# Kernel tuning notes

Hardware: AMD Instinct MI355X
Metric: run time of the kernel (lower is better)

The kernel has to match this reference:

```python
import jax, jax.numpy as jnp
import numpy as np

N_SRC = [700000, 51200, 5120]
N_DST = [51200, 5120, 1024]
N_EDGE = [768000, 51200, 5120]
IN_FEATS, N_HIDDEN, N_CLASSES = 128, 256, 47


def setup_inputs() -> dict:
    key = jax.random.key(0)
    ks = jax.random.split(key, 16)
    inp = {}
    inp["x"] = jax.random.normal(ks[0], (N_SRC[0], IN_FEATS), dtype=jnp.float32)
    # edge lists per block: src indexes block-src nodes, dst indexes block-dst nodes
    for l in range(3):
        inp[f"src{l}"] = jax.random.randint(ks[1 + 2 * l], (N_EDGE[l],), 0, N_SRC[l], dtype=jnp.int32)
        inp[f"dst{l}"] = jax.random.randint(ks[2 + 2 * l], (N_EDGE[l],), 0, N_DST[l], dtype=jnp.int32)
    dims = [(IN_FEATS, N_HIDDEN), (N_HIDDEN, N_HIDDEN), (N_HIDDEN, N_CLASSES)]
    for l, (di, do) in enumerate(dims):
        scale = 1.0 / np.sqrt(di)
        inp[f"Ws{l}"] = jax.random.normal(ks[7 + 3 * l], (di, do), dtype=jnp.float32) * scale
        inp[f"Wn{l}"] = jax.random.normal(ks[8 + 3 * l], (di, do), dtype=jnp.float32) * scale
        inp[f"b{l}"] = jnp.zeros((do,), dtype=jnp.float32)
    return inp


def _sage_conv(h, src, dst, n_dst, Ws, Wn, b):
    # mean-aggregate neighbor (src) features onto dst nodes, then dual linear
    h_dst = h[:n_dst]                                   # dst nodes are a prefix of src nodes
    msg = jax.ops.segment_sum(h[src], dst, num_segments=n_dst)
    deg = jax.ops.segment_sum(jnp.ones((src.shape[0], 1), h.dtype), dst, num_segments=n_dst)
    h_neigh = msg / jnp.maximum(deg, 1.0)               # zero-degree dst -> 0 (DGL convention)
    return h_dst @ Ws + h_neigh @ Wn + b


def reference(x, src0, dst0, src1, dst1, src2, dst2,
              Ws0, Wn0, b0, Ws1, Wn1, b1, Ws2, Wn2, b2):
    h = _sage_conv(x, src0, dst0, N_DST[0], Ws0, Wn0, b0)
    h = jax.nn.relu(h)  # dropout = identity in eval
    h = _sage_conv(h, src1, dst1, N_DST[1], Ws1, Wn1, b1)
    h = jax.nn.relu(h)
    h = _sage_conv(h, src2, dst2, N_DST[2], Ws2, Wn2, b2)
    return h
```

## Files before the change

kernel.cpp:

```cpp
#include <hip/hip_runtime.h>


typedef __bf16 bf16x8 __attribute__((ext_vector_type(8)));
typedef float f32x4 __attribute__((ext_vector_type(4)));

static __device__ __forceinline__ unsigned short f32_to_bf16(float f) {
    unsigned u = __float_as_uint(f);
    u += 0x7fffu + ((u >> 16) & 1u);
    return (unsigned short)(u >> 16);
}
static __device__ __forceinline__ float bf16lo(unsigned u) { return __uint_as_float(u << 16); }
static __device__ __forceinline__ float bf16hi(unsigned u) { return __uint_as_float(u & 0xffff0000u); }

__global__ void sage_prep(const float* __restrict__ x, unsigned short* __restrict__ xcast,
                          const float* __restrict__ Ws0, const float* __restrict__ Wn0,
                          const float* __restrict__ Ws1, const float* __restrict__ Wn1,
                          const float* __restrict__ Ws2, const float* __restrict__ Wn2,
                          unsigned short* __restrict__ WT0, unsigned short* __restrict__ WT1,
                          unsigned short* __restrict__ WT2,
                          const int* __restrict__ d0, int* __restrict__ c0,
                          const int* __restrict__ d1, int* __restrict__ c1,
                          const int* __restrict__ d2, int* __restrict__ c2) {
    const int b = blockIdx.x;
    if (b < 6400) {
        int i = b * 256 + threadIdx.x;
        float4 v = ((const float4*)x)[i];
        uint2 o;
        o.x = (unsigned)f32_to_bf16(v.x) | ((unsigned)f32_to_bf16(v.y) << 16);
        o.y = (unsigned)f32_to_bf16(v.z) | ((unsigned)f32_to_bf16(v.w) << 16);
        ((uint2*)xcast)[i] = o;
    } else if (b < 6656) {
        int idx = (b - 6400) * 256 + threadIdx.x;
        int n = idx >> 8, k = idx & 255;
        float v = (k < 128) ? Ws0[(size_t)k * 256 + n] : Wn0[(size_t)(k - 128) * 256 + n];
        WT0[idx] = f32_to_bf16(v);
    } else if (b < 7168) {
        int idx = (b - 6656) * 256 + threadIdx.x;
        int n = idx >> 9, k = idx & 511;
        float v = (k < 256) ? Ws1[(size_t)k * 256 + n] : Wn1[(size_t)(k - 256) * 256 + n];
        WT1[idx] = f32_to_bf16(v);
    } else if (b < 7262) {
        int idx = (b - 7168) * 256 + threadIdx.x;
        int n = idx >> 9, k = idx & 511;
        float v = (k < 256) ? Ws2[(size_t)k * 47 + n] : Wn2[(size_t)(k - 256) * 47 + n];
        WT2[idx] = f32_to_bf16(v);
    } else if (b < 8762) {
        int i = (b - 7262) * 256 + threadIdx.x;
        int2 d = ((const int2*)d0)[i];
        atomicAdd(&c0[d.x], 1);
        atomicAdd(&c0[d.y], 1);
    } else if (b < 8862) {
        int i = (b - 8762) * 256 + threadIdx.x;
        int2 d = ((const int2*)d1)[i];
        atomicAdd(&c1[d.x], 1);
        atomicAdd(&c1[d.y], 1);
    } else {
        int i = (b - 8862) * 256 + threadIdx.x;
        int2 d = ((const int2*)d2)[i];
        atomicAdd(&c2[d.x], 1);
        atomicAdd(&c2[d.y], 1);
    }
}

__launch_bounds__(1024)
__global__ void sage_scan(const int* __restrict__ c0, int* __restrict__ o0, int* __restrict__ u0,
                          const int* __restrict__ c1, int* __restrict__ o1, int* __restrict__ u1,
                          const int* __restrict__ c2, int* __restrict__ o2, int* __restrict__ u2,
                          int* __restrict__ sync) {
    const int b = blockIdx.x;
    const int tid = threadIdx.x;
    const int lane = tid & 63;
    const int wid = tid >> 6;
    const int* counts; int* off; int* cur; int chunk, first, nblk, n;
    if (b < 50)      { counts = c0; off = o0; cur = u0; chunk = b;      first = 0;  nblk = 50; n = 51200; }
    else if (b < 55) { counts = c1; off = o1; cur = u1; chunk = b - 50; first = 50; nblk = 5;  n = 5120;  }
    else             { counts = c2; off = o2; cur = u2; chunk = 0;      first = 55; nblk = 1;  n = 1024;  }

    const int idx = chunk * 1024 + tid;
    const int v = counts[idx];

    int incl = v;
#pragma unroll
    for (int d = 1; d < 64; d <<= 1) {
        int t = __shfl_up(incl, d, 64);
        if (lane >= d) incl += t;
    }

    __shared__ int wsum[16];
    __shared__ int s_base;
    if (lane == 63) wsum[wid] = incl;
    __syncthreads();

    if (tid < 64) {
        int s = (lane < 16) ? wsum[lane] : 0;
        int inc = s;
#pragma unroll
        for (int d = 1; d < 16; d <<= 1) {
            int t = __shfl_up(inc, d, 64);
            if (lane >= d) inc += t;
        }
        if (lane < 16) wsum[lane] = inc - s;
        if (lane == 15) {
            __hip_atomic_store(&sync[16 + b], inc, __ATOMIC_RELEASE, __HIP_MEMORY_SCOPE_AGENT);
            __hip_atomic_fetch_add(&sync[0], 1, __ATOMIC_RELEASE, __HIP_MEMORY_SCOPE_AGENT);
        }
    }
    if (tid == 0) {
        while (__hip_atomic_load(&sync[0], __ATOMIC_ACQUIRE, __HIP_MEMORY_SCOPE_AGENT) < 56)
            __builtin_amdgcn_s_sleep(2);
    }
    __syncthreads();

    if (tid < 64) {
        int p = (lane < chunk)
            ? __hip_atomic_load(&sync[16 + first + lane], __ATOMIC_RELAXED, __HIP_MEMORY_SCOPE_AGENT)
            : 0;
#pragma unroll
        for (int d = 32; d >= 1; d >>= 1) p += __shfl_down(p, d, 64);
        if (lane == 0) s_base = p;
    }
    __syncthreads();

    const int excl = s_base + wsum[wid] + (incl - v);
    off[idx] = excl;
    cur[idx] = excl;
    if (chunk == nblk - 1 && tid == 1023) off[n] = excl + v;
}

__global__ void sage_fill(const int* __restrict__ s0, const int* __restrict__ d0,
                          int* __restrict__ u0, int* __restrict__ r0,
                          const int* __restrict__ s1, const int* __restrict__ d1,
                          int* __restrict__ u1, int* __restrict__ r1,
                          const int* __restrict__ s2, const int* __restrict__ d2,
                          int* __restrict__ u2, int* __restrict__ r2) {
    const int b = blockIdx.x;
    if (b < 1500) {
        int i = b * 256 + threadIdx.x;
        int2 s = ((const int2*)s0)[i];
        int2 d = ((const int2*)d0)[i];
        int p0 = atomicAdd(&u0[d.x], 1);
        int p1 = atomicAdd(&u0[d.y], 1);
        r0[p0] = s.x;
        r0[p1] = s.y;
    } else if (b < 1600) {
        int i = (b - 1500) * 256 + threadIdx.x;
        int2 s = ((const int2*)s1)[i];
        int2 d = ((const int2*)d1)[i];
        int p0 = atomicAdd(&u1[d.x], 1);
        int p1 = atomicAdd(&u1[d.y], 1);
        r1[p0] = s.x;
        r1[p1] = s.y;
    } else {
        int i = (b - 1600) * 256 + threadIdx.x;
        int2 s = ((const int2*)s2)[i];
        int2 d = ((const int2*)d2)[i];
        int p0 = atomicAdd(&u2[d.x], 1);
        int p1 = atomicAdd(&u2[d.y], 1);
        r2[p0] = s.x;
        r2[p1] = s.y;
    }
}

__global__ void sage_gather0(const float* __restrict__ x, const int* __restrict__ csr,
                             const int* __restrict__ off, unsigned short* __restrict__ out,
                             int n_dst) {
    int row = (blockIdx.x * 256 + threadIdx.x) >> 6;
    if (row >= n_dst) return;
    const int lane = threadIdx.x & 63;
    const int half = lane >> 5;
    const int fl = lane & 31;
    const int beg = off[row], end = off[row + 1];
    const float4* hp = (const float4*)x + fl;
    float4 accA = make_float4(0.f, 0.f, 0.f, 0.f);
    float4 accB = make_float4(0.f, 0.f, 0.f, 0.f);
    int i = beg;
    for (; i + 7 < end; i += 8) {
        int s0 = csr[i + half];
        int s1 = csr[i + 2 + half];
        int s2 = csr[i + 4 + half];
        int s3 = csr[i + 6 + half];
        float4 v0 = hp[(size_t)s0 * 32];
        float4 v1 = hp[(size_t)s1 * 32];
        float4 v2 = hp[(size_t)s2 * 32];
        float4 v3 = hp[(size_t)s3 * 32];
        accA.x += v0.x; accA.y += v0.y; accA.z += v0.z; accA.w += v0.w;
        accB.x += v1.x; accB.y += v1.y; accB.z += v1.z; accB.w += v1.w;
        accA.x += v2.x; accA.y += v2.y; accA.z += v2.z; accA.w += v2.w;
        accB.x += v3.x; accB.y += v3.y; accB.z += v3.z; accB.w += v3.w;
    }
    for (; i + 1 < end; i += 2) {
        int s = csr[i + half];
        float4 v = hp[(size_t)s * 32];
        accA.x += v.x; accA.y += v.y; accA.z += v.z; accA.w += v.w;
    }
    if (i < end && half == 0) {
        int s = csr[i];
        float4 v = hp[(size_t)s * 32];
        accA.x += v.x; accA.y += v.y; accA.z += v.z; accA.w += v.w;
    }
    accA.x += accB.x; accA.y += accB.y; accA.z += accB.z; accA.w += accB.w;
    accA.x += __shfl_down(accA.x, 32);
    accA.y += __shfl_down(accA.y, 32);
    accA.z += __shfl_down(accA.z, 32);
    accA.w += __shfl_down(accA.w, 32);
    if (half == 0) {
        float inv = 1.0f / fmaxf((float)(end - beg), 1.0f);
        uint2 o;
        o.x = (unsigned)f32_to_bf16(accA.x * inv) | ((unsigned)f32_to_bf16(accA.y * inv) << 16);
        o.y = (unsigned)f32_to_bf16(accA.z * inv) | ((unsigned)f32_to_bf16(accA.w * inv) << 16);
        ((uint2*)out)[(size_t)row * 32 + fl] = o;
    }
}

__global__ void sage_gather256(const unsigned short* __restrict__ h, const int* __restrict__ csr,
                               const int* __restrict__ off, unsigned short* __restrict__ out,
                               int n_dst) {
    int row = (blockIdx.x * 256 + threadIdx.x) >> 6;
    if (row >= n_dst) return;
    const int lane = threadIdx.x & 63;
    const int half = lane >> 5;
    const int fl = lane & 31;
    const int beg = off[row], end = off[row + 1];
    const uint4* hp = (const uint4*)h + fl;
    float a[8] = {0.f, 0.f, 0.f, 0.f, 0.f, 0.f, 0.f, 0.f};
    float b[8] = {0.f, 0.f, 0.f, 0.f, 0.f, 0.f, 0.f, 0.f};
    int i = beg;
    for (; i + 3 < end; i += 4) {
        int s0 = csr[i + half];
        int s1 = csr[i + 2 + half];
        uint4 u0 = hp[(size_t)s0 * 32];
        uint4 u1 = hp[(size_t)s1 * 32];
        a[0] += bf16lo(u0.x); a[1] += bf16hi(u0.x);
        a[2] += bf16lo(u0.y); a[3] += bf16hi(u0.y);
        a[4] += bf16lo(u0.z); a[5] += bf16hi(u0.z);
        a[6] += bf16lo(u0.w); a[7] += bf16hi(u0.w);
        b[0] += bf16lo(u1.x); b[1] += bf16hi(u1.x);
        b[2] += bf16lo(u1.y); b[3] += bf16hi(u1.y);
        b[4] += bf16lo(u1.z); b[5] += bf16hi(u1.z);
        b[6] += bf16lo(u1.w); b[7] += bf16hi(u1.w);
    }
    for (; i + 1 < end; i += 2) {
        int s = csr[i + half];
        uint4 u = hp[(size_t)s * 32];
        a[0] += bf16lo(u.x); a[1] += bf16hi(u.x);
        a[2] += bf16lo(u.y); a[3] += bf16hi(u.y);
        a[4] += bf16lo(u.z); a[5] += bf16hi(u.z);
        a[6] += bf16lo(u.w); a[7] += bf16hi(u.w);
    }
    if (i < end && half == 0) {
        int s = csr[i];
        uint4 u = hp[(size_t)s * 32];
        a[0] += bf16lo(u.x); a[1] += bf16hi(u.x);
        a[2] += bf16lo(u.y); a[3] += bf16hi(u.y);
        a[4] += bf16lo(u.z); a[5] += bf16hi(u.z);
        a[6] += bf16lo(u.w); a[7] += bf16hi(u.w);
    }
#pragma unroll
    for (int k = 0; k < 8; ++k) { a[k] += b[k]; a[k] += __shfl_down(a[k], 32); }
    if (half == 0) {
        float inv = 1.0f / fmaxf((float)(end - beg), 1.0f);
        uint4 o;
        o.x = (unsigned)f32_to_bf16(a[0] * inv) | ((unsigned)f32_to_bf16(a[1] * inv) << 16);
        o.y = (unsigned)f32_to_bf16(a[2] * inv) | ((unsigned)f32_to_bf16(a[3] * inv) << 16);
        o.z = (unsigned)f32_to_bf16(a[4] * inv) | ((unsigned)f32_to_bf16(a[5] * inv) << 16);
        o.w = (unsigned)f32_to_bf16(a[6] * inv) | ((unsigned)f32_to_bf16(a[7] * inv) << 16);
        ((uint4*)out)[(size_t)row * 32 + fl] = o;
    }
}

template <int RELU, int OUT_BF16>
__launch_bounds__(256)
__global__ void sage_gemm(const unsigned short* __restrict__ Hdst,
                          const unsigned short* __restrict__ Hneigh,
                          const unsigned short* __restrict__ WT,
                          const float* __restrict__ bias,
                          void* __restrict__ Out,
                          int N, int K1) {
    const int Ktot = 2 * K1;
    __shared__ unsigned short smem[2][128][72];
    unsigned short (*As)[72] = smem[0];
    unsigned short (*Bs)[72] = smem[1];

    const int t = threadIdx.x;
    const int lane = t & 63;
    const int w = t >> 6;
    const int wm = (w >> 1) * 64;
    const int wn = (w & 1) * 64;
    const int bm = blockIdx.y * 128;
    const int bn = blockIdx.x * 128;

    const int rowL = t >> 1;
    const int kL = (t & 1) * 32;

    f32x4 acc[4][4] = {};

    const int ktiles = Ktot >> 6;
    for (int kt = 0; kt < ktiles; ++kt) {
        const int k0 = kt << 6;
        {
            const unsigned short* src = (k0 < K1)
                ? (Hdst + (size_t)(bm + rowL) * K1 + k0 + kL)
                : (Hneigh + (size_t)(bm + rowL) * K1 + (k0 - K1) + kL);
            uint4 v0 = *(const uint4*)src;
            uint4 v1 = *(const uint4*)(src + 8);
            uint4 v2 = *(const uint4*)(src + 16);
            uint4 v3 = *(const uint4*)(src + 24);
            *(uint4*)&As[rowL][kL]      = v0;
            *(uint4*)&As[rowL][kL + 8]  = v1;
            *(uint4*)&As[rowL][kL + 16] = v2;
            *(uint4*)&As[rowL][kL + 24] = v3;
        }
        {
            int n = bn + rowL;
            uint4 v0 = {0,0,0,0}, v1 = {0,0,0,0}, v2 = {0,0,0,0}, v3 = {0,0,0,0};
            if (n < N) {
                const unsigned short* srcB = WT + (size_t)n * Ktot + k0 + kL;
                v0 = *(const uint4*)srcB;
                v1 = *(const uint4*)(srcB + 8);
                v2 = *(const uint4*)(srcB + 16);
                v3 = *(const uint4*)(srcB + 24);
            }
            *(uint4*)&Bs[rowL][kL]      = v0;
            *(uint4*)&Bs[rowL][kL + 8]  = v1;
            *(uint4*)&Bs[rowL][kL + 16] = v2;
            *(uint4*)&Bs[rowL][kL + 24] = v3;
        }
        __syncthreads();

        const int fr = lane & 15;
        const int fk = (lane >> 4) * 8;
#pragma unroll
        for (int ks = 0; ks < 64; ks += 32) {
            bf16x8 av[4], bv[4];
#pragma unroll
            for (int mt = 0; mt < 4; ++mt) av[mt] = *(const bf16x8*)&As[wm + mt * 16 + fr][ks + fk];
#pragma unroll
            for (int nt = 0; nt < 4; ++nt) bv[nt] = *(const bf16x8*)&Bs[wn + nt * 16 + fr][ks + fk];
#pragma unroll
            for (int mt = 0; mt < 4; ++mt)
#pragma unroll
                for (int nt = 0; nt < 4; ++nt)
                    acc[mt][nt] = __builtin_amdgcn_mfma_f32_16x16x32_bf16(av[mt], bv[nt], acc[mt][nt], 0, 0, 0);
        }
        __syncthreads();
    }

    const int quad = lane >> 4;
    const int colL = lane & 15;
    if (OUT_BF16 && N == 256) {
        unsigned short* C = (unsigned short*)smem;
#pragma unroll
        for (int mt = 0; mt < 4; ++mt)
#pragma unroll
            for (int nt = 0; nt < 4; ++nt)
#pragma unroll
                for (int r = 0; r < 4; ++r) {
                    int lrow = wm + mt * 16 + quad * 4 + r;
                    int lcol = wn + nt * 16 + colL;
                    float v = acc[mt][nt][r] + bias[bn + lcol];
                    if (RELU) v = fmaxf(v, 0.0f);
                    C[lrow * 136 + lcol] = f32_to_bf16(v);
                }
        __syncthreads();
        unsigned short* o = (unsigned short*)Out;
#pragma unroll
        for (int c = 0; c < 8; ++c) {
            int chunk = t * 8 + c;
            int row = chunk >> 4, cc = chunk & 15;
            uint4 v = *(const uint4*)&C[row * 136 + cc * 8];
            *(uint4*)(o + (size_t)(bm + row) * N + bn + cc * 8) = v;
        }
    } else {
#pragma unroll
        for (int mt = 0; mt < 4; ++mt)
#pragma unroll
            for (int nt = 0; nt < 4; ++nt)
#pragma unroll
                for (int r = 0; r < 4; ++r) {
                    int grow = bm + wm + mt * 16 + quad * 4 + r;
                    int gcol = bn + wn + nt * 16 + colL;
                    if (gcol < N) {
                        float v = acc[mt][nt][r] + bias[gcol];
                        if (RELU) v = fmaxf(v, 0.0f);
                        if (OUT_BF16) ((unsigned short*)Out)[(size_t)grow * N + gcol] = f32_to_bf16(v);
                        else ((float*)Out)[(size_t)grow * N + gcol] = v;
                    }
                }
    }
}


extern "C" void kernel_launch(void* const* d_in, const int* in_sizes, int n_in,
                              void* d_out, int out_size, void* d_ws, size_t ws_size,
                              hipStream_t stream) {
    const float* x    = (const float*)d_in[0];
    const int* src0 = (const int*)d_in[1];
    const int* dst0 = (const int*)d_in[2];
    const int* src1 = (const int*)d_in[3];
    const int* dst1 = (const int*)d_in[4];
    const int* src2 = (const int*)d_in[5];
    const int* dst2 = (const int*)d_in[6];
    const float* Ws0 = (const float*)d_in[7];
    const float* Wn0 = (const float*)d_in[8];
    const float* b0  = (const float*)d_in[9];
    const float* Ws1 = (const float*)d_in[10];
    const float* Wn1 = (const float*)d_in[11];
    const float* b1  = (const float*)d_in[12];
    const float* Ws2 = (const float*)d_in[13];
    const float* Wn2 = (const float*)d_in[14];
    const float* b2  = (const float*)d_in[15];
    float* out = (float*)d_out;

    char* ws = (char*)d_ws;
    unsigned short* xcast   = (unsigned short*)(ws + 0);
    unsigned short* h1      = (unsigned short*)(ws + 13107200);
    unsigned short* h2      = (unsigned short*)(ws + 39321600);
    unsigned short* hneigh0 = (unsigned short*)(ws + 41943040);
    unsigned short* hneigh1 = (unsigned short*)(ws + 55050240);
    unsigned short* hneigh2 = (unsigned short*)(ws + 57671680);
    unsigned short* WT0     = (unsigned short*)(ws + 58195968);
    unsigned short* WT1     = (unsigned short*)(ws + 58327040);
    unsigned short* WT2     = (unsigned short*)(ws + 58589184);
    int* counts0 = (int*)(ws + 58637312);
    int* counts1 = (int*)(ws + 58842112);
    int* counts2 = (int*)(ws + 58862592);
    int* syncp   = (int*)(ws + 58866688);
    int* off0    = (int*)(ws + 58870784);
    int* off1    = (int*)(ws + 59075600);
    int* off2    = (int*)(ws + 59096096);
    int* cur0    = (int*)(ws + 59100208);
    int* cur1    = (int*)(ws + 59305008);
    int* cur2    = (int*)(ws + 59325488);
    int* csr0    = (int*)(ws + 59329584);
    int* csr1    = (int*)(ws + 62401584);
    int* csr2    = (int*)(ws + 62606384);

    hipMemsetAsync(counts0, 0, 233472, stream);

    sage_prep<<<8872, 256, 0, stream>>>(x, xcast, Ws0, Wn0, Ws1, Wn1, Ws2, Wn2,
                                        WT0, WT1, WT2,
                                        dst0, counts0, dst1, counts1, dst2, counts2);
    sage_scan<<<56, 1024, 0, stream>>>(counts0, off0, cur0, counts1, off1, cur1,
                                       counts2, off2, cur2, syncp);
    sage_fill<<<1610, 256, 0, stream>>>(src0, dst0, cur0, csr0,
                                        src1, dst1, cur1, csr1,
                                        src2, dst2, cur2, csr2);

    sage_gather0<<<12800, 256, 0, stream>>>(x, csr0, off0, hneigh0, 51200);
    { dim3 g(2, 400); sage_gemm<1, 1><<<g, 256, 0, stream>>>(xcast, hneigh0, WT0, b0, h1, 256, 128); }

    sage_gather256<<<1280, 256, 0, stream>>>(h1, csr1, off1, hneigh1, 5120);
    { dim3 g(2, 40); sage_gemm<1, 1><<<g, 256, 0, stream>>>(h1, hneigh1, WT1, b1, h2, 256, 256); }

    sage_gather256<<<256, 256, 0, stream>>>(h2, csr2, off2, hneigh2, 1024);
    { dim3 g(1, 8); sage_gemm<0, 0><<<g, 256, 0, stream>>>(h2, hneigh2, WT2, b2, out, 47, 256); }
}
```

Measured before the change: 652.9 us.

## Fuse scan with CSR fill via grid barrier; use direct global-to-LDS loads in GEMM

Merges the prefix-scan and CSR fill kernels into one 56-block kernel. A second atomic grid barrier sits between the two phases, and the fill runs as a grid-stride loop, removing one launch. The GEMM now stages A/B tiles with global_load_lds 16-byte copies into an XOR-swizzled unpadded LDS layout, and clamps out-of-range B rows instead of zero-filling them. The fill now runs on only 56 blocks, which lowers parallelism for the atomic scatter. The barrier also relies on all 56 blocks being co-resident.

```diff
diff --git a/kernel.cpp b/kernel.cpp
--- a/kernel.cpp
+++ b/kernel.cpp
@@ -11,6 +11,11 @@
 }
 static __device__ __forceinline__ float bf16lo(unsigned u) { return __uint_as_float(u << 16); }
 static __device__ __forceinline__ float bf16hi(unsigned u) { return __uint_as_float(u & 0xffff0000u); }
+
+static __device__ __forceinline__ void gl_lds16(const unsigned short* g, unsigned short* l) {
+    __builtin_amdgcn_global_load_lds((const __attribute__((address_space(1))) void*)g,
+                                     (__attribute__((address_space(3))) void*)l, 16, 0, 0);
+}
 
 __global__ void sage_prep(const float* __restrict__ x, unsigned short* __restrict__ xcast,
                           const float* __restrict__ Ws0, const float* __restrict__ Wn0,
@@ -63,10 +68,13 @@
 }
 
 __launch_bounds__(1024)
-__global__ void sage_scan(const int* __restrict__ c0, int* __restrict__ o0, int* __restrict__ u0,
-                          const int* __restrict__ c1, int* __restrict__ o1, int* __restrict__ u1,
-                          const int* __restrict__ c2, int* __restrict__ o2, int* __restrict__ u2,
-                          int* __restrict__ sync) {
+__global__ void sage_scanfill(const int* __restrict__ c0, int* __restrict__ o0, int* __restrict__ u0,
+                              const int* __restrict__ c1, int* __restrict__ o1, int* __restrict__ u1,
+                              const int* __restrict__ c2, int* __restrict__ o2, int* __restrict__ u2,
+                              int* __restrict__ sync,
+                              const int* __restrict__ s0, const int* __restrict__ d0, int* __restrict__ r0,
+                              const int* __restrict__ s1, const int* __restrict__ d1, int* __restrict__ r1,
+                              const int* __restrict__ s2, const int* __restrict__ d2, int* __restrict__ r2) {
     const int b = blockIdx.x;
     const int tid = threadIdx.x;
     const int lane = tid & 63;
@@ -123,41 +131,29 @@
 
     const int excl = s_base + wsum[wid] + (incl - v);
     off[idx] = excl;
-    cur[idx] = excl;
+    __hip_atomic_store(&cur[idx], excl, __ATOMIC_RELAXED, __HIP_MEMORY_SCOPE_AGENT);
     if (chunk == nblk - 1 && tid == 1023) off[n] = excl + v;
-}
-
-__global__ void sage_fill(const int* __restrict__ s0, const int* __restrict__ d0,
-                          int* __restrict__ u0, int* __restrict__ r0,
-                          const int* __restrict__ s1, const int* __restrict__ d1,
-                          int* __restrict__ u1, int* __restrict__ r1,
-                          const int* __restrict__ s2, const int* __restrict__ d2,
-                          int* __restrict__ u2, int* __restrict__ r2) {
-    const int b = blockIdx.x;
-    if (b < 1500) {
-        int i = b * 256 + threadIdx.x;
-        int2 s = ((const int2*)s0)[i];
-        int2 d = ((const int2*)d0)[i];
-        int p0 = atomicAdd(&u0[d.x], 1);
-        int p1 = atomicAdd(&u0[d.y], 1);
-        r0[p0] = s.x;
-        r0[p1] = s.y;
-    } else if (b < 1600) {
-        int i = (b - 1500) * 256 + threadIdx.x;
-        int2 s = ((const int2*)s1)[i];
-        int2 d = ((const int2*)d1)[i];
-        int p0 = atomicAdd(&u1[d.x], 1);
-        int p1 = atomicAdd(&u1[d.y], 1);
-        r1[p0] = s.x;
-        r1[p1] = s.y;
-    } else {
-        int i = (b - 1600) * 256 + threadIdx.x;
-        int2 s = ((const int2*)s2)[i];
-        int2 d = ((const int2*)d2)[i];
-        int p0 = atomicAdd(&u2[d.x], 1);
-        int p1 = atomicAdd(&u2[d.y], 1);
-        r2[p0] = s.x;
-        r2[p1] = s.y;
+
+    __syncthreads();
+    if (tid == 0) {
+        __hip_atomic_fetch_add(&sync[1], 1, __ATOMIC_RELEASE, __HIP_MEMORY_SCOPE_AGENT);
+        while (__hip_atomic_load(&sync[1], __ATOMIC_ACQUIRE, __HIP_MEMORY_SCOPE_AGENT) < 56)
+            __builtin_amdgcn_s_sleep(2);
+    }
+    __syncthreads();
+
+    const int gtid = b * 1024 + tid;
+    for (int i = gtid; i < 412160; i += 57344) {
+        const int* sp; const int* dp; int* up; int* rp; int ii;
+        if (i < 384000)      { sp = s0; dp = d0; up = u0; rp = r0; ii = i; }
+        else if (i < 409600) { sp = s1; dp = d1; up = u1; rp = r1; ii = i - 384000; }
+        else                 { sp = s2; dp = d2; up = u2; rp = r2; ii = i - 409600; }
+        int2 s = ((const int2*)sp)[ii];
+        int2 d = ((const int2*)dp)[ii];
+        int p0 = atomicAdd(&up[d.x], 1);
+        int p1 = atomicAdd(&up[d.y], 1);
+        rp[p0] = s.x;
+        rp[p1] = s.y;
     }
 }
 
@@ -277,9 +273,9 @@
                           void* __restrict__ Out,
                           int N, int K1) {
     const int Ktot = 2 * K1;
-    __shared__ unsigned short smem[2][128][72];
-    unsigned short (*As)[72] = smem[0];
-    unsigned short (*Bs)[72] = smem[1];
+    __shared__ unsigned short smem[17408];
+    unsigned short (*As)[64] = (unsigned short(*)[64])smem;
+    unsigned short (*Bs)[64] = (unsigned short(*)[64])(smem + 8192);
 
     const int t = threadIdx.x;
     const int lane = t & 63;
@@ -289,53 +285,46 @@
     const int bm = blockIdx.y * 128;
     const int bn = blockIdx.x * 128;
 
-    const int rowL = t >> 1;
-    const int kL = (t & 1) * 32;
+    const int srow = (w << 5) + (lane >> 3);
+    const int scol = ((lane & 7) ^ (lane >> 3)) << 3;
+    const int sdst = w << 5;
 
     f32x4 acc[4][4] = {};
 
     const int ktiles = Ktot >> 6;
     for (int kt = 0; kt < ktiles; ++kt) {
         const int k0 = kt << 6;
-        {
-            const unsigned short* src = (k0 < K1)
-                ? (Hdst + (size_t)(bm + rowL) * K1 + k0 + kL)
-                : (Hneigh + (size_t)(bm + rowL) * K1 + (k0 - K1) + kL);
-            uint4 v0 = *(const uint4*)src;
-            uint4 v1 = *(const uint4*)(src + 8);
-            uint4 v2 = *(const uint4*)(src + 16);
-            uint4 v3 = *(const uint4*)(src + 24);
-            *(uint4*)&As[rowL][kL]      = v0;
-            *(uint4*)&As[rowL][kL + 8]  = v1;
-            *(uint4*)&As[rowL][kL + 16] = v2;
-            *(uint4*)&As[rowL][kL + 24] = v3;
-        }
-        {
-            int n = bn + rowL;
-            uint4 v0 = {0,0,0,0}, v1 = {0,0,0,0}, v2 = {0,0,0,0}, v3 = {0,0,0,0};
-            if (n < N) {
-                const unsigned short* srcB = WT + (size_t)n * Ktot + k0 + kL;
-                v0 = *(const uint4*)srcB;
-                v1 = *(const uint4*)(srcB + 8);
-                v2 = *(const uint4*)(srcB + 16);
-                v3 = *(const uint4*)(srcB + 24);
+        const unsigned short* baseA = (k0 < K1) ? (Hdst + k0) : (Hneigh + (k0 - K1));
+#pragma unroll
+        for (int j = 0; j < 4; ++j) {
+            const unsigned short* g = baseA + (size_t)(bm + srow + j * 8) * K1 + scol;
+            gl_lds16(g, &As[sdst + j * 8][0]);
+        }
+#pragma unroll
+        for (int j = 0; j < 4; ++j) {
+            int nr = bn + srow + j * 8;
+            if (nr > N - 1) nr = N - 1;
+            const unsigned short* g = WT + (size_t)nr * Ktot + k0 + scol;
+            gl_lds16(g, &Bs[sdst + j * 8][0]);
+        }
+        __syncthreads();
+
+        const int fr = lane & 15;
+        const int fq = lane >> 4;
+#pragma unroll
+        for (int ks = 0; ks < 64; ks += 32) {
+            const int c = (ks >> 3) + fq;
+            bf16x8 av[4], bv[4];
+#pragma unroll
+            for (int mt = 0; mt < 4; ++mt) {
+                int r = wm + mt * 16 + fr;
+                av[mt] = *(const bf16x8*)&As[r][(c ^ (r & 7)) << 3];
             }
-            *(uint4*)&Bs[rowL][kL]      = v0;
-            *(uint4*)&Bs[rowL][kL + 8]  = v1;
-            *(uint4*)&Bs[rowL][kL + 16] = v2;
-            *(uint4*)&Bs[rowL][kL + 24] = v3;
-        }
-        __syncthreads();
-
-        const int fr = lane & 15;
-        const int fk = (lane >> 4) * 8;
-#pragma unroll
-        for (int ks = 0; ks < 64; ks += 32) {
-            bf16x8 av[4], bv[4];
-#pragma unroll
-            for (int mt = 0; mt < 4; ++mt) av[mt] = *(const bf16x8*)&As[wm + mt * 16 + fr][ks + fk];
-#pragma unroll
-            for (int nt = 0; nt < 4; ++nt) bv[nt] = *(const bf16x8*)&Bs[wn + nt * 16 + fr][ks + fk];
+#pragma unroll
+            for (int nt = 0; nt < 4; ++nt) {
+                int r = wn + nt * 16 + fr;
+                bv[nt] = *(const bf16x8*)&Bs[r][(c ^ (r & 7)) << 3];
+            }
 #pragma unroll
             for (int mt = 0; mt < 4; ++mt)
 #pragma unroll
@@ -348,7 +337,7 @@
     const int quad = lane >> 4;
     const int colL = lane & 15;
     if (OUT_BF16 && N == 256) {
-        unsigned short* C = (unsigned short*)smem;
+        unsigned short* C = smem;
 #pragma unroll
         for (int mt = 0; mt < 4; ++mt)
 #pragma unroll
@@ -440,11 +429,11 @@
     sage_prep<<<8872, 256, 0, stream>>>(x, xcast, Ws0, Wn0, Ws1, Wn1, Ws2, Wn2,
                                         WT0, WT1, WT2,
                                         dst0, counts0, dst1, counts1, dst2, counts2);
-    sage_scan<<<56, 1024, 0, stream>>>(counts0, off0, cur0, counts1, off1, cur1,
-                                       counts2, off2, cur2, syncp);
-    sage_fill<<<1610, 256, 0, stream>>>(src0, dst0, cur0, csr0,
-                                        src1, dst1, cur1, csr1,
-                                        src2, dst2, cur2, csr2);
+    sage_scanfill<<<56, 1024, 0, stream>>>(counts0, off0, cur0, counts1, off1, cur1,
+                                           counts2, off2, cur2, syncp,
+                                           src0, dst0, csr0,
+                                           src1, dst1, csr1,
+                                           src2, dst2, csr2);
 
     sage_gather0<<<12800, 256, 0, stream>>>(x, csr0, off0, hneigh0, 51200);
     { dim3 g(2, 400); sage_gemm<1, 1><<<g, 256, 0, stream>>>(xcast, hneigh0, WT0, b0, h1, 256, 128); }
```

Measured after the change: 663.3 us. No clear change (+1.6%).
